# Optimization experiments

Hardware: AMD Instinct MI355X
Metric: run time of the kernel (lower is better)

Reference implementation:

```python
import jax, jax.numpy as jnp
import numpy as np

N = 100000   # num nodes
E = 1200000  # num edges
D = 64       # num_features
H = 64       # hidden_channels
P = 0.5      # dropout prob


def setup_inputs() -> dict:
    key = jax.random.key(0)
    ks = jax.random.split(key, 9)
    x = jax.random.normal(ks[0], (N, D), dtype=jnp.float32)
    edge_index = jax.random.randint(ks[1], (2, E), 0, N, dtype=jnp.int64)
    u1 = jax.random.uniform(ks[2], (N, H), dtype=jnp.float32)  # dropout uniforms

    def glorot(k, shape):
        fan = shape[0]
        return jax.random.normal(k, shape, dtype=jnp.float32) / jnp.sqrt(jnp.float32(fan))

    W1_l = glorot(ks[3], (D, H))  # weight on aggregated neighbors
    W1_r = glorot(ks[4], (D, H))  # root (self) weight
    b1 = jnp.zeros((H,), jnp.float32)
    W2_l = glorot(ks[5], (H, H))
    W2_r = glorot(ks[6], (H, H))
    b2 = jnp.zeros((H,), jnp.float32)
    return {"x": x, "edge_index": edge_index, "u1": u1,
            "W1_l": W1_l, "W1_r": W1_r, "b1": b1,
            "W2_l": W2_l, "W2_r": W2_r, "b2": b2}


def sage_conv(h, edge_index, W_l, W_r, b):
    # SAGEConv (mean aggregation, root weight, bias)
    src, dst = edge_index[0], edge_index[1]
    msg = h[src]                                            # [E, C] gather
    agg = jax.ops.segment_sum(msg, dst, num_segments=N)     # [N, C] scatter-add
    cnt = jax.ops.segment_sum(jnp.ones((E, 1), h.dtype), dst, num_segments=N)
    mean = agg / jnp.maximum(cnt, 1.0)                      # mean over in-neighbors
    return mean @ W_l + h @ W_r + b


def reference(x, edge_index, u1, W1_l, W1_r, b1, W2_l, W2_r, b2):
    h = jax.nn.relu(sage_conv(x, edge_index, W1_l, W1_r, b1))
    # dropout (training=True), deterministic mask from u1
    mask = (u1 > P).astype(h.dtype) / (1.0 - P)
    h = h * mask
    h = jax.nn.relu(sage_conv(h, edge_index, W2_l, W2_r, b2))
    return h
```

## Files before the change

### kernel.cpp

```cpp
#include <hip/hip_runtime.h>
#include <hip/hip_bf16.h>

#define N_NODES 100000
#define N_EDGES 1200000
#define DIM 64
#define NBUCK ((N_NODES + 127) / 128)
#define HCHUNK 4096
#define NBIN_H ((N_EDGES + HCHUNK - 1) / HCHUNK)
#define BCHUNK 8192
#define NBIN_B ((N_EDGES + BCHUNK - 1) / BCHUNK)

static __device__ __forceinline__ unsigned short bf16bits(float f) {
    __hip_bfloat16 h = __float2bfloat16(f);
    return *reinterpret_cast<unsigned short*>(&h);
}
static __device__ __forceinline__ float bf16raw2f(unsigned short s) {
    return __uint_as_float(((unsigned)s) << 16);
}

__global__ __launch_bounds__(256) void hist_kernel(const int* __restrict__ dst,
                                                   int* __restrict__ bcnt) {
    __shared__ int lb[NBUCK];
    for (int i = threadIdx.x; i < NBUCK; i += 256) lb[i] = 0;
    __syncthreads();
    const int e0 = blockIdx.x * HCHUNK;
    const int e1 = min(e0 + HCHUNK, N_EDGES);
    for (int e = e0 + threadIdx.x; e < e1; e += 256)
        atomicAdd(&lb[dst[e] >> 7], 1);
    __syncthreads();
    for (int i = threadIdx.x; i < NBUCK; i += 256) {
        int c = lb[i];
        if (c) atomicAdd(&bcnt[i], c);
    }
}

__global__ __launch_bounds__(1024) void bucket_scan_kernel(const int* __restrict__ bcnt,
                                                           int* __restrict__ boff,
                                                           int* __restrict__ bcur,
                                                           int* __restrict__ noff) {
    __shared__ int tmp[1024];
    const int t = threadIdx.x;
    int v = (t < NBUCK) ? bcnt[t] : 0;
    tmp[t] = v;
    __syncthreads();
    for (int ofs = 1; ofs < 1024; ofs <<= 1) {
        int x = (t >= ofs) ? tmp[t - ofs] : 0;
        __syncthreads();
        tmp[t] += x;
        __syncthreads();
    }
    if (t < NBUCK) {
        int ex = tmp[t] - v;
        boff[t] = ex;
        bcur[t] = ex;
    }
    if (t == 0) noff[N_NODES] = N_EDGES;
}

__global__ __launch_bounds__(256) void bin_kernel(const int* __restrict__ src,
                                                  const int* __restrict__ dst,
                                                  int* __restrict__ bcur,
                                                  unsigned* __restrict__ tmp) {
    __shared__ int lcnt[NBUCK];
    __shared__ int lbase[NBUCK];
    const int tid = threadIdx.x;
    for (int i = tid; i < NBUCK; i += 256) lcnt[i] = 0;
    __syncthreads();
    const int e0 = blockIdx.x * BCHUNK;
    const int e1 = min(e0 + BCHUNK, N_EDGES);
    for (int e = e0 + tid; e < e1; e += 256)
        atomicAdd(&lcnt[dst[e] >> 7], 1);
    __syncthreads();
    for (int i = tid; i < NBUCK; i += 256) {
        int c = lcnt[i];
        lbase[i] = c ? atomicAdd(&bcur[i], c) : 0;
    }
    __syncthreads();
    for (int i = tid; i < NBUCK; i += 256) lcnt[i] = 0;
    __syncthreads();
    for (int e = e0 + tid; e < e1; e += 256) {
        int d = dst[e];
        int b = d >> 7;
        int r = atomicAdd(&lcnt[b], 1);
        tmp[lbase[b] + r] = ((unsigned)(d & 127) << 17) | (unsigned)src[e];
    }
}

__global__ __launch_bounds__(256) void bucket_sort_kernel(
    const unsigned* __restrict__ tmp,
    const int* __restrict__ boff,
    const int* __restrict__ bcnt,
    int* __restrict__ noff,
    int* __restrict__ ssrc) {
    __shared__ int lcnt[128];
    __shared__ int lofs[128];
    const int tid = threadIdx.x;
    const int b = blockIdx.x;
    const int start = boff[b];
    const int len = bcnt[b];

    if (tid < 128) lcnt[tid] = 0;
    __syncthreads();
    for (int i = tid; i < len; i += 256)
        atomicAdd(&lcnt[tmp[start + i] >> 17], 1);
    __syncthreads();
    if (tid < 128) lofs[tid] = lcnt[tid];
    __syncthreads();
    for (int ofs = 1; ofs < 128; ofs <<= 1) {
        int v = (tid < 128 && tid >= ofs) ? lofs[tid - ofs] : 0;
        __syncthreads();
        if (tid < 128) lofs[tid] += v;
        __syncthreads();
    }
    if (tid < 128) {
        int ex = lofs[tid] - lcnt[tid];
        int n = b * 128 + tid;
        if (n < N_NODES) noff[n] = start + ex;
        lcnt[tid] = ex;
    }
    __syncthreads();
    for (int i = tid; i < len; i += 256) {
        unsigned v = tmp[start + i];
        int d = v >> 17;
        int r = atomicAdd(&lcnt[d], 1);
        ssrc[start + r] = (int)(v & 0x1FFFFu);
    }
}

__global__ __launch_bounds__(256) void cvt_bf16_kernel(const float* __restrict__ in,
                                                       unsigned short* __restrict__ out) {
    int i = blockIdx.x * blockDim.x + threadIdx.x;
    const int total = N_NODES * DIM / 4;
    if (i >= total) return;
    float4 v = ((const float4*)in)[i];
    ushort4 p;
    p.x = bf16bits(v.x); p.y = bf16bits(v.y); p.z = bf16bits(v.z); p.w = bf16bits(v.w);
    ((ushort4*)out)[i] = p;
}

__global__ __launch_bounds__(256) void aggregate_bf16_kernel(
    const unsigned short* __restrict__ hb,
    const int* __restrict__ ssrc,
    const int* __restrict__ noff,
    float* __restrict__ mean) {
    const int lane = threadIdx.x & 63;
    const int wave = (blockIdx.x * blockDim.x + threadIdx.x) >> 6;
    if (wave >= N_NODES) return;
    const int n = wave;
    const int start = noff[n];
    const int end = noff[n + 1];
    const int deg = end - start;
    const int half = lane >> 5;
    const int fl = lane & 31;

    float acc0 = 0.0f, acc1 = 0.0f;
    for (int base = start; base < end; base += 64) {
        const int m = min(64, end - base);
        int idx = (lane < m) ? ssrc[base + lane] : 0;
        const int npair = m >> 1;
        int i = 0;
        for (; i + 4 <= npair; i += 4) {
            unsigned v[4];
#pragma unroll
            for (int k = 0; k < 4; ++k) {
                int s = __shfl(idx, 2 * (i + k) + half, 64);
                v[k] = *(const unsigned*)(hb + (size_t)s * DIM + fl * 2);
            }
#pragma unroll
            for (int k = 0; k < 4; ++k) {
                acc0 += bf16raw2f((unsigned short)(v[k] & 0xFFFFu));
                acc1 += bf16raw2f((unsigned short)(v[k] >> 16));
            }
        }
        for (; i < npair; ++i) {
            int s = __shfl(idx, 2 * i + half, 64);
            unsigned v = *(const unsigned*)(hb + (size_t)s * DIM + fl * 2);
            acc0 += bf16raw2f((unsigned short)(v & 0xFFFFu));
            acc1 += bf16raw2f((unsigned short)(v >> 16));
        }
        if (m & 1) {
            int s = __shfl(idx, m - 1, 64);
            if (half == 0) {
                unsigned v = *(const unsigned*)(hb + (size_t)s * DIM + fl * 2);
                acc0 += bf16raw2f((unsigned short)(v & 0xFFFFu));
                acc1 += bf16raw2f((unsigned short)(v >> 16));
            }
        }
    }
    float t0 = acc0 + __shfl(acc0, fl + 32, 64);
    float t1 = acc1 + __shfl(acc1, fl + 32, 64);
    if (half == 0) {
        float inv = 1.0f / fmaxf((float)deg, 1.0f);
        float2 w;
        w.x = t0 * inv;
        w.y = t1 * inv;
        *(float2*)(mean + (size_t)n * DIM + fl * 2) = w;
    }
}

__global__ __launch_bounds__(256) void aggregate_f32_kernel(
    const float* __restrict__ h,
    const int* __restrict__ ssrc,
    const int* __restrict__ noff,
    float* __restrict__ mean) {
    const int lane = threadIdx.x & 63;
    const int wave = (blockIdx.x * blockDim.x + threadIdx.x) >> 6;
    if (wave >= N_NODES) return;
    const int n = wave;
    const int start = noff[n];
    const int end = noff[n + 1];
    const int deg = end - start;

    float acc = 0.0f;
    for (int base = start; base < end; base += 64) {
        const int m = min(64, end - base);
        int idx = (lane < m) ? ssrc[base + lane] : 0;
        int i = 0;
        for (; i + 8 <= m; i += 8) {
            float v[8];
#pragma unroll
            for (int k = 0; k < 8; ++k) {
                int s = __shfl(idx, i + k, 64);
                v[k] = h[(size_t)s * DIM + lane];
            }
            acc += ((v[0] + v[1]) + (v[2] + v[3])) + ((v[4] + v[5]) + (v[6] + v[7]));
        }
        for (; i < m; ++i) {
            int s = __shfl(idx, i, 64);
            acc += h[(size_t)s * DIM + lane];
        }
    }
    mean[(size_t)n * DIM + lane] = acc / fmaxf((float)deg, 1.0f);
}

template <int LAYER, int SELFB>
__global__ __launch_bounds__(256) void combine_kernel(
    const float* __restrict__ mean,
    const float* __restrict__ hf,
    const unsigned short* __restrict__ hb,
    const float* __restrict__ Wl,
    const float* __restrict__ Wr,
    const float* __restrict__ bias,
    const float* __restrict__ u1,
    float* __restrict__ outf,
    unsigned short* __restrict__ outb) {
    const int lane = threadIdx.x & 63;
    const int wv = __builtin_amdgcn_readfirstlane((int)(threadIdx.x >> 6));
    const int j0 = wv * 16;
    const int n0 = blockIdx.x * 64 + lane;
    const int n = (n0 < N_NODES) ? n0 : (N_NODES - 1);
    const bool ok = (n0 < N_NODES);

    float acc[16];
#pragma unroll
    for (int j = 0; j < 16; ++j) acc[j] = bias[j0 + j];

    const float* mrow = mean + (size_t)n * DIM;
#pragma unroll
    for (int kc = 0; kc < DIM; kc += 4) {
        float4 am = *(const float4*)(mrow + kc);
        float a4[4] = {am.x, am.y, am.z, am.w};
#pragma unroll
        for (int kk = 0; kk < 4; ++kk) {
#pragma unroll
            for (int j = 0; j < 16; ++j)
                acc[j] += a4[kk] * Wl[(kc + kk) * DIM + j0 + j];
        }
    }

    if (SELFB == 0) {
        const float* hrow = hf + (size_t)n * DIM;
#pragma unroll
        for (int kc = 0; kc < DIM; kc += 4) {
            float4 ah = *(const float4*)(hrow + kc);
            float a4[4] = {ah.x, ah.y, ah.z, ah.w};
#pragma unroll
            for (int kk = 0; kk < 4; ++kk) {
#pragma unroll
                for (int j = 0; j < 16; ++j)
                    acc[j] += a4[kk] * Wr[(kc + kk) * DIM + j0 + j];
            }
        }
    } else {
        const unsigned short* hrow = hb + (size_t)n * DIM;
#pragma unroll
        for (int kc = 0; kc < DIM; kc += 8) {
            union { uint4 q; unsigned short s[8]; } u;
            u.q = *(const uint4*)(hrow + kc);
#pragma unroll
            for (int kk = 0; kk < 8; ++kk) {
                float a = bf16raw2f(u.s[kk]);
#pragma unroll
                for (int j = 0; j < 16; ++j)
                    acc[j] += a * Wr[(kc + kk) * DIM + j0 + j];
            }
        }
    }

#pragma unroll
    for (int j = 0; j < 16; ++j) acc[j] = fmaxf(acc[j], 0.0f);

    if (LAYER == 1) {
        const float* urow = u1 + (size_t)n * DIM + j0;
#pragma unroll
        for (int jc = 0; jc < 16; jc += 4) {
            float4 u4 = *(const float4*)(urow + jc);
            float uv[4] = {u4.x, u4.y, u4.z, u4.w};
#pragma unroll
            for (int t = 0; t < 4; ++t)
                acc[jc + t] = (uv[t] > 0.5f) ? acc[jc + t] * 2.0f : 0.0f;
        }
        if (ok) {
#pragma unroll
            for (int jc = 0; jc < 16; jc += 4) {
                ushort4 p;
                p.x = bf16bits(acc[jc]);
                p.y = bf16bits(acc[jc + 1]);
                p.z = bf16bits(acc[jc + 2]);
                p.w = bf16bits(acc[jc + 3]);
                *(ushort4*)(outb + (size_t)n * DIM + j0 + jc) = p;
            }
        }
    } else {
        if (ok) {
#pragma unroll
            for (int jc = 0; jc < 16; jc += 4) {
                float4 v;
                v.x = acc[jc]; v.y = acc[jc + 1]; v.z = acc[jc + 2]; v.w = acc[jc + 3];
                *(float4*)(outf + (size_t)n * DIM + j0 + jc) = v;
            }
        }
    }
}

extern "C" void kernel_launch(void* const* d_in, const int* in_sizes, int n_in,
                              void* d_out, int out_size, void* d_ws, size_t ws_size,
                              hipStream_t stream) {
    const float* x   = (const float*)d_in[0];
    const int*   ei  = (const int*)d_in[1];
    const float* u1  = (const float*)d_in[2];
    const float* W1l = (const float*)d_in[3];
    const float* W1r = (const float*)d_in[4];
    const float* b1  = (const float*)d_in[5];
    const float* W2l = (const float*)d_in[6];
    const float* W2r = (const float*)d_in[7];
    const float* b2  = (const float*)d_in[8];
    float* out = (float*)d_out;

    const int* src = ei;
    const int* dst = ei + N_EDGES;

    char* ws = (char*)d_ws;
    auto align256 = [](size_t v) { return (v + 255) & ~(size_t)255; };
    size_t o = 0;
    int* noff = (int*)(ws + o); o = align256(o + (size_t)(N_NODES + 1) * 4);
    int* bcnt = (int*)(ws + o); size_t zeroB = (size_t)NBUCK * 4; o = align256(o + zeroB);
    int* boff = (int*)(ws + o); o = align256(o + (size_t)NBUCK * 4);
    int* bcur = (int*)(ws + o); o = align256(o + (size_t)NBUCK * 4);
    int* ssrc = (int*)(ws + o); o = align256(o + (size_t)N_EDGES * 4);
    float* mean = (float*)(ws + o); o = align256(o + (size_t)N_NODES * DIM * 4);
    unsigned* tmp = (unsigned*)mean;
    unsigned short* h1b = (unsigned short*)(ws + o); o = align256(o + (size_t)N_NODES * DIM * 2);
    unsigned short* xb  = (unsigned short*)(ws + o);
    size_t need_xb = o + (size_t)N_NODES * DIM * 2;
    const bool useXb = (ws_size >= need_xb);

    hipMemsetAsync(bcnt, 0, zeroB, stream);

    const int cbBlocks = (N_NODES + 63) / 64;
    const int cvBlocks = (N_NODES * DIM / 4 + 255) / 256;
    const int aggBlocks = (N_NODES + 3) / 4;

    hist_kernel<<<NBIN_H, 256, 0, stream>>>(dst, bcnt);
    bucket_scan_kernel<<<1, 1024, 0, stream>>>(bcnt, boff, bcur, noff);
    bin_kernel<<<NBIN_B, 256, 0, stream>>>(src, dst, bcur, tmp);
    bucket_sort_kernel<<<NBUCK, 256, 0, stream>>>(tmp, boff, bcnt, noff, ssrc);

    if (useXb) {
        cvt_bf16_kernel<<<cvBlocks, 256, 0, stream>>>(x, xb);
        aggregate_bf16_kernel<<<aggBlocks, 256, 0, stream>>>(xb, ssrc, noff, mean);
        combine_kernel<1, 1><<<cbBlocks, 256, 0, stream>>>(mean, nullptr, xb, W1l, W1r, b1,
                                                           u1, nullptr, h1b);
    } else {
        aggregate_f32_kernel<<<aggBlocks, 256, 0, stream>>>(x, ssrc, noff, mean);
        combine_kernel<1, 0><<<cbBlocks, 256, 0, stream>>>(mean, x, nullptr, W1l, W1r, b1,
                                                           u1, nullptr, h1b);
    }

    aggregate_bf16_kernel<<<aggBlocks, 256, 0, stream>>>(h1b, ssrc, noff, mean);
    combine_kernel<2, 1><<<cbBlocks, 256, 0, stream>>>(mean, nullptr, h1b, W2l, W2r, b2,
                                                       nullptr, out, nullptr);
}
```

Measured before the change: 323.4 us.

## Use bf16 MFMA for SAGE combine with transposed bf16 weights and bf16 means

Replaces the scalar FP32 combine kernel with a matrix-core kernel that uses 16x16x32 bf16 MFMA, concatenating the mean and self features along K against a pre-transposed bf16 weight matrix. The aggregation now writes the mean in bf16, halving that intermediate's traffic. Histogram and binning chunk sizes are reduced to launch more blocks, and the FP32 fallback path is removed. In exchange, precision drops from bf16 rounding of the means and weights, and output stores become scattered scalar writes.

```diff
diff --git a/kernel.cpp b/kernel.cpp
--- a/kernel.cpp
+++ b/kernel.cpp
@@ -5,10 +5,13 @@
 #define N_EDGES 1200000
 #define DIM 64
 #define NBUCK ((N_NODES + 127) / 128)
-#define HCHUNK 4096
+#define HCHUNK 2048
 #define NBIN_H ((N_EDGES + HCHUNK - 1) / HCHUNK)
-#define BCHUNK 8192
+#define BCHUNK 2048
 #define NBIN_B ((N_EDGES + BCHUNK - 1) / BCHUNK)
+
+typedef __attribute__((ext_vector_type(8))) short bf16x8;
+typedef __attribute__((ext_vector_type(4))) float f32x4;
 
 static __device__ __forceinline__ unsigned short bf16bits(float f) {
     __hip_bfloat16 h = __float2bfloat16(f);
@@ -138,11 +141,28 @@
     ((ushort4*)out)[i] = p;
 }
 
+__global__ __launch_bounds__(256) void cvt_wt_kernel(const float* __restrict__ W1l,
+                                                     const float* __restrict__ W1r,
+                                                     const float* __restrict__ W2l,
+                                                     const float* __restrict__ W2r,
+                                                     unsigned short* __restrict__ w1t,
+                                                     unsigned short* __restrict__ w2t) {
+    const float* Wl = blockIdx.x ? W2l : W1l;
+    const float* Wr = blockIdx.x ? W2r : W1r;
+    unsigned short* wt = blockIdx.x ? w2t : w1t;
+    for (int i = threadIdx.x; i < 64 * 128; i += 256) {
+        int c = i >> 7;
+        int k = i & 127;
+        float v = (k < 64) ? Wl[k * 64 + c] : Wr[(k - 64) * 64 + c];
+        wt[c * 128 + k] = bf16bits(v);
+    }
+}
+
 __global__ __launch_bounds__(256) void aggregate_bf16_kernel(
     const unsigned short* __restrict__ hb,
     const int* __restrict__ ssrc,
     const int* __restrict__ noff,
-    float* __restrict__ mean) {
+    unsigned short* __restrict__ meanb) {
     const int lane = threadIdx.x & 63;
     const int wave = (blockIdx.x * blockDim.x + threadIdx.x) >> 6;
     if (wave >= N_NODES) return;
@@ -191,143 +211,59 @@
     float t1 = acc1 + __shfl(acc1, fl + 32, 64);
     if (half == 0) {
         float inv = 1.0f / fmaxf((float)deg, 1.0f);
-        float2 w;
-        w.x = t0 * inv;
-        w.y = t1 * inv;
-        *(float2*)(mean + (size_t)n * DIM + fl * 2) = w;
-    }
-}
-
-__global__ __launch_bounds__(256) void aggregate_f32_kernel(
-    const float* __restrict__ h,
-    const int* __restrict__ ssrc,
-    const int* __restrict__ noff,
-    float* __restrict__ mean) {
-    const int lane = threadIdx.x & 63;
-    const int wave = (blockIdx.x * blockDim.x + threadIdx.x) >> 6;
-    if (wave >= N_NODES) return;
-    const int n = wave;
-    const int start = noff[n];
-    const int end = noff[n + 1];
-    const int deg = end - start;
-
-    float acc = 0.0f;
-    for (int base = start; base < end; base += 64) {
-        const int m = min(64, end - base);
-        int idx = (lane < m) ? ssrc[base + lane] : 0;
-        int i = 0;
-        for (; i + 8 <= m; i += 8) {
-            float v[8];
-#pragma unroll
-            for (int k = 0; k < 8; ++k) {
-                int s = __shfl(idx, i + k, 64);
-                v[k] = h[(size_t)s * DIM + lane];
-            }
-            acc += ((v[0] + v[1]) + (v[2] + v[3])) + ((v[4] + v[5]) + (v[6] + v[7]));
-        }
-        for (; i < m; ++i) {
-            int s = __shfl(idx, i, 64);
-            acc += h[(size_t)s * DIM + lane];
-        }
-    }
-    mean[(size_t)n * DIM + lane] = acc / fmaxf((float)deg, 1.0f);
-}
-
-template <int LAYER, int SELFB>
-__global__ __launch_bounds__(256) void combine_kernel(
-    const float* __restrict__ mean,
-    const float* __restrict__ hf,
-    const unsigned short* __restrict__ hb,
-    const float* __restrict__ Wl,
-    const float* __restrict__ Wr,
+        unsigned pk = ((unsigned)bf16bits(t1 * inv) << 16) | (unsigned)bf16bits(t0 * inv);
+        *(unsigned*)(meanb + (size_t)n * DIM + fl * 2) = pk;
+    }
+}
+
+template <int LAYER>
+__global__ __launch_bounds__(256) void combine_mfma_kernel(
+    const unsigned short* __restrict__ meanb,
+    const unsigned short* __restrict__ selfb,
+    const unsigned short* __restrict__ WT,
     const float* __restrict__ bias,
     const float* __restrict__ u1,
     float* __restrict__ outf,
     unsigned short* __restrict__ outb) {
     const int lane = threadIdx.x & 63;
-    const int wv = __builtin_amdgcn_readfirstlane((int)(threadIdx.x >> 6));
-    const int j0 = wv * 16;
-    const int n0 = blockIdx.x * 64 + lane;
-    const int n = (n0 < N_NODES) ? n0 : (N_NODES - 1);
-    const bool ok = (n0 < N_NODES);
-
-    float acc[16];
+    const int wid = (blockIdx.x * blockDim.x + threadIdx.x) >> 6;
+    const int n0 = wid * 16;
+    if (n0 >= N_NODES) return;
+    const int rl = lane & 15;
+    const int kg = lane >> 4;
+
+    const size_t arow = (size_t)(n0 + rl) * DIM;
+    bf16x8 a0 = *(const bf16x8*)(meanb + arow + 0 + kg * 8);
+    bf16x8 a1 = *(const bf16x8*)(meanb + arow + 32 + kg * 8);
+    bf16x8 a2 = *(const bf16x8*)(selfb + arow + 0 + kg * 8);
+    bf16x8 a3 = *(const bf16x8*)(selfb + arow + 32 + kg * 8);
+
 #pragma unroll
-    for (int j = 0; j < 16; ++j) acc[j] = bias[j0 + j];
-
-    const float* mrow = mean + (size_t)n * DIM;
+    for (int ct = 0; ct < 4; ++ct) {
+        const int col = ct * 16 + rl;
+        const unsigned short* wcol = WT + (size_t)col * 128 + kg * 8;
+        bf16x8 b0 = *(const bf16x8*)(wcol + 0);
+        bf16x8 b1 = *(const bf16x8*)(wcol + 32);
+        bf16x8 b2 = *(const bf16x8*)(wcol + 64);
+        bf16x8 b3 = *(const bf16x8*)(wcol + 96);
+        float bv = bias[col];
+        f32x4 acc = {bv, bv, bv, bv};
+        acc = __builtin_amdgcn_mfma_f32_16x16x32_bf16(a0, b0, acc, 0, 0, 0);
+        acc = __builtin_amdgcn_mfma_f32_16x16x32_bf16(a1, b1, acc, 0, 0, 0);
+        acc = __builtin_amdgcn_mfma_f32_16x16x32_bf16(a2, b2, acc, 0, 0, 0);
+        acc = __builtin_amdgcn_mfma_f32_16x16x32_bf16(a3, b3, acc, 0, 0, 0);
+
+        const int rowb = n0 + kg * 4;
 #pragma unroll
-    for (int kc = 0; kc < DIM; kc += 4) {
-        float4 am = *(const float4*)(mrow + kc);
-        float a4[4] = {am.x, am.y, am.z, am.w};
-#pragma unroll
-        for (int kk = 0; kk < 4; ++kk) {
-#pragma unroll
-            for (int j = 0; j < 16; ++j)
-                acc[j] += a4[kk] * Wl[(kc + kk) * DIM + j0 + j];
-        }
-    }
-
-    if (SELFB == 0) {
-        const float* hrow = hf + (size_t)n * DIM;
-#pragma unroll
-        for (int kc = 0; kc < DIM; kc += 4) {
-            float4 ah = *(const float4*)(hrow + kc);
-            float a4[4] = {ah.x, ah.y, ah.z, ah.w};
-#pragma unroll
-            for (int kk = 0; kk < 4; ++kk) {
-#pragma unroll
-                for (int j = 0; j < 16; ++j)
-                    acc[j] += a4[kk] * Wr[(kc + kk) * DIM + j0 + j];
-            }
-        }
-    } else {
-        const unsigned short* hrow = hb + (size_t)n * DIM;
-#pragma unroll
-        for (int kc = 0; kc < DIM; kc += 8) {
-            union { uint4 q; unsigned short s[8]; } u;
-            u.q = *(const uint4*)(hrow + kc);
-#pragma unroll
-            for (int kk = 0; kk < 8; ++kk) {
-                float a = bf16raw2f(u.s[kk]);
-#pragma unroll
-                for (int j = 0; j < 16; ++j)
-                    acc[j] += a * Wr[(kc + kk) * DIM + j0 + j];
-            }
-        }
-    }
-
-#pragma unroll
-    for (int j = 0; j < 16; ++j) acc[j] = fmaxf(acc[j], 0.0f);
-
-    if (LAYER == 1) {
-        const float* urow = u1 + (size_t)n * DIM + j0;
-#pragma unroll
-        for (int jc = 0; jc < 16; jc += 4) {
-            float4 u4 = *(const float4*)(urow + jc);
-            float uv[4] = {u4.x, u4.y, u4.z, u4.w};
-#pragma unroll
-            for (int t = 0; t < 4; ++t)
-                acc[jc + t] = (uv[t] > 0.5f) ? acc[jc + t] * 2.0f : 0.0f;
-        }
-        if (ok) {
-#pragma unroll
-            for (int jc = 0; jc < 16; jc += 4) {
-                ushort4 p;
-                p.x = bf16bits(acc[jc]);
-                p.y = bf16bits(acc[jc + 1]);
-                p.z = bf16bits(acc[jc + 2]);
-                p.w = bf16bits(acc[jc + 3]);
-                *(ushort4*)(outb + (size_t)n * DIM + j0 + jc) = p;
-            }
-        }
-    } else {
-        if (ok) {
-#pragma unroll
-            for (int jc = 0; jc < 16; jc += 4) {
-                float4 v;
-                v.x = acc[jc]; v.y = acc[jc + 1]; v.z = acc[jc + 2]; v.w = acc[jc + 3];
-                *(float4*)(outf + (size_t)n * DIM + j0 + jc) = v;
+        for (int r = 0; r < 4; ++r) {
+            float v = fmaxf(acc[r], 0.0f);
+            const size_t oidx = (size_t)(rowb + r) * DIM + col;
+            if (LAYER == 1) {
+                float u = u1[oidx];
+                v = (u > 0.5f) ? v * 2.0f : 0.0f;
+                outb[oidx] = bf16bits(v);
+            } else {
+                outf[oidx] = v;
             }
         }
     }
@@ -357,17 +293,17 @@
     int* bcnt = (int*)(ws + o); size_t zeroB = (size_t)NBUCK * 4; o = align256(o + zeroB);
     int* boff = (int*)(ws + o); o = align256(o + (size_t)NBUCK * 4);
     int* bcur = (int*)(ws + o); o = align256(o + (size_t)NBUCK * 4);
+    unsigned short* w1t = (unsigned short*)(ws + o); o = align256(o + (size_t)64 * 128 * 2);
+    unsigned short* w2t = (unsigned short*)(ws + o); o = align256(o + (size_t)64 * 128 * 2);
     int* ssrc = (int*)(ws + o); o = align256(o + (size_t)N_EDGES * 4);
-    float* mean = (float*)(ws + o); o = align256(o + (size_t)N_NODES * DIM * 4);
-    unsigned* tmp = (unsigned*)mean;
+    unsigned short* meanb = (unsigned short*)(ws + o); o = align256(o + (size_t)N_NODES * DIM * 2);
+    unsigned* tmp = (unsigned*)meanb;
     unsigned short* h1b = (unsigned short*)(ws + o); o = align256(o + (size_t)N_NODES * DIM * 2);
-    unsigned short* xb  = (unsigned short*)(ws + o);
-    size_t need_xb = o + (size_t)N_NODES * DIM * 2;
-    const bool useXb = (ws_size >= need_xb);
+    unsigned short* xb  = (unsigned short*)(ws + o); o += (size_t)N_NODES * DIM * 2;
 
     hipMemsetAsync(bcnt, 0, zeroB, stream);
 
-    const int cbBlocks = (N_NODES + 63) / 64;
+    const int cbBlocks = (N_NODES / 16 + 3) / 4;
     const int cvBlocks = (N_NODES * DIM / 4 + 255) / 256;
     const int aggBlocks = (N_NODES + 3) / 4;
 
@@ -376,18 +312,14 @@
     bin_kernel<<<NBIN_B, 256, 0, stream>>>(src, dst, bcur, tmp);
     bucket_sort_kernel<<<NBUCK, 256, 0, stream>>>(tmp, boff, bcnt, noff, ssrc);
 
-    if (useXb) {
-        cvt_bf16_kernel<<<cvBlocks, 256, 0, stream>>>(x, xb);
-        aggregate_bf16_kernel<<<aggBlocks, 256, 0, stream>>>(xb, ssrc, noff, mean);
-        combine_kernel<1, 1><<<cbBlocks, 256, 0, stream>>>(mean, nullptr, xb, W1l, W1r, b1,
-                                                           u1, nullptr, h1b);
-    } else {
-        aggregate_f32_kernel<<<aggBlocks, 256, 0, stream>>>(x, ssrc, noff, mean);
-        combine_kernel<1, 0><<<cbBlocks, 256, 0, stream>>>(mean, x, nullptr, W1l, W1r, b1,
-                                                           u1, nullptr, h1b);
-    }
-
-    aggregate_bf16_kernel<<<aggBlocks, 256, 0, stream>>>(h1b, ssrc, noff, mean);
-    combine_kernel<2, 1><<<cbBlocks, 256, 0, stream>>>(mean, nullptr, h1b, W2l, W2r, b2,
-                                                       nullptr, out, nullptr);
-}
+    cvt_bf16_kernel<<<cvBlocks, 256, 0, stream>>>(x, xb);
+    cvt_wt_kernel<<<2, 256, 0, stream>>>(W1l, W1r, W2l, W2r, w1t, w2t);
+
+    aggregate_bf16_kernel<<<aggBlocks, 256, 0, stream>>>(xb, ssrc, noff, meanb);
+    combine_mfma_kernel<1><<<cbBlocks, 256, 0, stream>>>(meanb, xb, w1t, b1, u1,
+                                                         nullptr, h1b);
+
+    aggregate_bf16_kernel<<<aggBlocks, 256, 0, stream>>>(h1b, ssrc, noff, meanb);
+    combine_mfma_kernel<2><<<cbBlocks, 256, 0, stream>>>(meanb, h1b, w2t, b2, nullptr,
+                                                         out, nullptr);
+}
```

Measured after the change: 294.0 us. -9.1%, faster.
